# Optimization experiments

Hardware: AMD Instinct MI355X
Metric: run time of the kernel (lower is better)

The kernel has to match this reference:

```python
import jax, jax.numpy as jnp
import numpy as np

HEAD = 8

def setup_inputs() -> dict:
    key = jax.random.key(0)
    ks = jax.random.split(key, 11)
    B, C, W, H = 16, 512, 32, 32
    d, N = C // HEAD, W * H
    return {
        "x": jax.random.normal(ks[0], (B, C, W, H), jnp.float32),
        "Wq": jax.random.normal(ks[1], (C, C), jnp.float32) * 0.02,
        "bq": jax.random.normal(ks[2], (C,), jnp.float32) * 0.02,
        "Wk": jax.random.normal(ks[3], (C, C), jnp.float32) * 0.02,
        "bk": jax.random.normal(ks[4], (C,), jnp.float32) * 0.02,
        "Wv": jax.random.normal(ks[5], (C, C), jnp.float32) * 0.02,
        "bv": jax.random.normal(ks[6], (C,), jnp.float32) * 0.02,
        "rel_h": jax.random.normal(ks[7], (1, HEAD, d, 1, H), jnp.float32),
        "rel_w": jax.random.normal(ks[8], (1, HEAD, d, W, 1), jnp.float32),
        "reg_qk": jax.random.normal(ks[9], (1, N, N), jnp.float32),
        "reg_v": jax.random.normal(ks[10], (1, d, N), jnp.float32),
    }

def reference(x, Wq, bq, Wk, bk, Wv, bv, rel_h, rel_w, reg_qk, reg_v):
    B, C, W, H = x.shape
    head = HEAD
    d = C // head
    N = W * H
    def conv1x1(inp, Wt, b):  # 1x1 conv == per-pixel linear
        return jnp.einsum('bchw,oc->bohw', inp, Wt) + b[None, :, None, None]
    q = conv1x1(x, Wq, bq).reshape(B, head, d, N)
    k = conv1x1(x, Wk, bk).reshape(B, head, d, N)
    v = conv1x1(x, Wv, bv).reshape(B, head, d, N)
    # content-content: q^T k -> [B, head, N, N]
    cc = jnp.einsum('bhdn,bhdm->bhnm', q, k)
    # content-position: (rel_h + rel_w) broadcast to [1, head, d, W, H] -> [head, N, d]
    pos = (rel_h + rel_w).reshape(head, d, N)
    cp = jnp.einsum('hdn,bhdm->bhnm', pos, q)
    energy = cc + cp  # [B, head, N, N]
    n_reg = reg_qk.shape[0]
    energy = jnp.concatenate(
        [energy, jnp.broadcast_to(reg_qk[None], (B, n_reg, N, N))], axis=1)
    v_all = jnp.concatenate(
        [v, jnp.broadcast_to(reg_v[None], (B, n_reg, d, N))], axis=1)
    attn = jax.nn.softmax(energy, axis=-1)  # [B, head+n_reg, N, N]
    # v @ attn^T
    out = jnp.einsum('bgdn,bgmn->bgdm', v_all, attn)
    out = out[:, :head].reshape(B, C, W, H)
    return out + x
```

## Files before the change

### kernel.cpp

```cpp
#include <hip/hip_runtime.h>

#define BB   16
#define HEADS 8
#define DH   64
#define NSP  1024
#define CCH  512

typedef unsigned int   u32;
typedef unsigned short u16;
typedef __attribute__((ext_vector_type(8))) short  short8;
typedef __attribute__((ext_vector_type(4))) float  floatx4;

#if defined(__has_builtin)
#if __has_builtin(__builtin_amdgcn_exp2f)
#define EXP2F(x) __builtin_amdgcn_exp2f(x)
#else
#define EXP2F(x) exp2f(x)
#endif
#else
#define EXP2F(x) exp2f(x)
#endif

__device__ __forceinline__ u16 f2b(float f) {
  u32 x = __float_as_uint(f);
  x = x + 0x7fffu + ((x >> 16) & 1u);
  return (u16)(x >> 16);
}

__device__ __forceinline__ u32 pkbf(float lo, float hi) {
  return __builtin_amdgcn_perm(__float_as_uint(hi) + 0x8000u,
                               __float_as_uint(lo) + 0x8000u, 0x07060302u);
}

__device__ __forceinline__ void gload_lds16(const u16* g, u16* l) {
  __builtin_amdgcn_global_load_lds((const __attribute__((address_space(1))) u32*)g,
                                   (__attribute__((address_space(3))) u32*)l, 16, 0, 0);
}

__global__ __launch_bounds__(256) void prep_wcast(const float* __restrict__ Wq,
                                                  const float* __restrict__ Wk,
                                                  const float* __restrict__ Wv,
                                                  u16* __restrict__ wbf) {
  int idx = blockIdx.x * 256 + threadIdx.x;
  int which = idx >> 16;
  int r4 = (idx & 65535) * 4;
  const float* src = which == 0 ? Wq : which == 1 ? Wk : Wv;
  float4 v = *(const float4*)&src[r4];
  ushort4 s;
  s.x = f2b(v.x); s.y = f2b(v.y); s.z = f2b(v.z); s.w = f2b(v.w);
  *(ushort4*)&wbf[(which << 18) + r4] = s;
}

__global__ __launch_bounds__(256) void prep_pos(const float* __restrict__ rel_h,
                                                const float* __restrict__ rel_w,
                                                u16* __restrict__ pos) {
  int idx = blockIdx.x * 256 + threadIdx.x;
  int dd = idx & 63;
  int n  = (idx >> 6) & 1023;
  int h  = idx >> 16;
  int ww = n >> 5, hh = n & 31;
  float v = rel_h[(h * 64 + dd) * 32 + hh] + rel_w[(h * 64 + dd) * 32 + ww];
  pos[idx] = f2b(v);
}

__global__ __launch_bounds__(256) void prep_xt(const float* __restrict__ x,
                                               u16* __restrict__ xt) {
  int ntile = blockIdx.x, ctile = blockIdx.y, b = blockIdx.z;
  __shared__ float ld[64][68];
  int t = threadIdx.x;
  const float* xb = x + (((size_t)b * CCH + ctile * 64) << 10) + ntile * 64;
#pragma unroll
  for (int p = 0; p < 4; ++p) {
    int c = p * 16 + (t >> 4), n4 = (t & 15) * 4;
    float4 v = *(const float4*)&xb[((size_t)c << 10) + n4];
    ld[c][n4 + 0] = v.x; ld[c][n4 + 1] = v.y; ld[c][n4 + 2] = v.z; ld[c][n4 + 3] = v.w;
  }
  __syncthreads();
  u16* xo = xt + (((size_t)b << 10) + ntile * 64) * CCH + ctile * 64;
#pragma unroll
  for (int p = 0; p < 2; ++p) {
    int id = p * 256 + t;
    int n = id >> 3, c8 = (id & 7) * 8;
    ushort4 s0, s1;
    s0.x = f2b(ld[c8 + 0][n]); s0.y = f2b(ld[c8 + 1][n]);
    s0.z = f2b(ld[c8 + 2][n]); s0.w = f2b(ld[c8 + 3][n]);
    s1.x = f2b(ld[c8 + 4][n]); s1.y = f2b(ld[c8 + 5][n]);
    s1.z = f2b(ld[c8 + 6][n]); s1.w = f2b(ld[c8 + 7][n]);
    *(ushort4*)&xo[(size_t)n * CCH + c8] = s0;
    *(ushort4*)&xo[(size_t)n * CCH + c8 + 4] = s1;
  }
}

__global__ __launch_bounds__(256, 3) void qkv_mfma(const u16* __restrict__ wbf,
                                                   const u16* __restrict__ xt,
                                                   const float* __restrict__ bq,
                                                   const float* __restrict__ bk,
                                                   const float* __restrict__ bv,
                                                   u16* __restrict__ qw,
                                                   u16* __restrict__ kw,
                                                   u16* __restrict__ vtw) {
  int ntile = blockIdx.x, otile = blockIdx.y;
  int b = blockIdx.z & 15, which = blockIdx.z >> 4;
  int o0 = otile * 128, n0 = ntile * 128;

  __shared__ __align__(16) u16 At[128 * 64];
  __shared__ __align__(16) u16 Bt[128 * 64];

  int t = threadIdx.x;
  int w = t >> 6, lane = t & 63;
  int l15 = lane & 15, quad = lane >> 4;
  int wrM = (w >> 1) * 64, wrN = (w & 1) * 64;

  const u16* Ag = wbf + ((size_t)which << 18) + (size_t)o0 * CCH;
  const u16* Bg = xt + (((size_t)b << 10) + n0) * CCH;

  floatx4 acc[4][4];
#pragma unroll
  for (int i = 0; i < 4; ++i)
#pragma unroll
    for (int j = 0; j < 4; ++j) acc[i][j] = (floatx4){0.f, 0.f, 0.f, 0.f};

  const u16* aSrc = which == 2 ? Bt : At;
  const u16* bSrc = which == 2 ? At : Bt;

  int srow = lane >> 3;
  int scc = ((lane & 7) ^ srow) << 3;

  for (int k0 = 0; k0 < CCH; k0 += 64) {
    __syncthreads();
#pragma unroll
    for (int p = 0; p < 4; ++p) {
      int r0 = (w * 4 + p) * 8;
      int row = r0 + srow;
      gload_lds16(Ag + (size_t)row * CCH + k0 + scc, &At[r0 * 64]);
      gload_lds16(Bg + (size_t)row * CCH + k0 + scc, &Bt[r0 * 64]);
    }
    __syncthreads();
#pragma unroll
    for (int ks = 0; ks < 2; ++ks) {
      short8 af[4], bf4[4];
#pragma unroll
      for (int s = 0; s < 4; ++s) {
        int ra = wrM + s * 16 + l15;
        int rb = wrN + s * 16 + l15;
        af[s]  = *(const short8*)&aSrc[ra * 64 + (((ks * 4 + quad) ^ (ra & 7)) << 3)];
        bf4[s] = *(const short8*)&bSrc[rb * 64 + (((ks * 4 + quad) ^ (rb & 7)) << 3)];
      }
#pragma unroll
      for (int i = 0; i < 4; ++i)
#pragma unroll
        for (int j = 0; j < 4; ++j)
          acc[i][j] = __builtin_amdgcn_mfma_f32_16x16x32_bf16(af[i], bf4[j], acc[i][j], 0, 0, 0);
    }
  }

  if (which == 2) {
#pragma unroll
    for (int i = 0; i < 4; ++i) {
      int n = n0 + wrM + i * 16 + quad * 4;
      int nt = n >> 6, nn = n & 63;
#pragma unroll
      for (int j = 0; j < 4; ++j) {
        int o = o0 + wrN + j * 16 + l15;
        int h = o >> 6, dd = o & 63;
        float bias = bv[o];
        uint2 s;
        s.x = pkbf(acc[i][j][0] + bias, acc[i][j][1] + bias);
        s.y = pkbf(acc[i][j][2] + bias, acc[i][j][3] + bias);
        *(uint2*)&vtw[(((size_t)(b * HEADS + h) * 16 + nt) * 64 + dd) * 64 + nn] = s;
      }
    }
  } else {
    const float* bias = which == 0 ? bq : bk;
    u16* dst = which == 0 ? qw : kw;
#pragma unroll
    for (int i = 0; i < 4; ++i) {
      int o = o0 + wrM + i * 16 + quad * 4;
      int h = o >> 6, dd = o & 63;
      float b0 = bias[o], b1 = bias[o + 1], b2 = bias[o + 2], b3 = bias[o + 3];
      size_t hb = (size_t)(b * HEADS + h) * NSP;
#pragma unroll
      for (int j = 0; j < 4; ++j) {
        int n = n0 + wrN + j * 16 + l15;
        uint2 s;
        s.x = pkbf(acc[i][j][0] + b0, acc[i][j][1] + b1);
        s.y = pkbf(acc[i][j][2] + b2, acc[i][j][3] + b3);
        *(uint2*)&dst[(hb + n) * 64 + dd] = s;
      }
    }
  }
}

__global__ __launch_bounds__(256, 2) void attn_mfma(const u16* __restrict__ qw,
                                                    const u16* __restrict__ kw,
                                                    const u16* __restrict__ vtw,
                                                    const u16* __restrict__ pos,
                                                    const float* __restrict__ x,
                                                    float* __restrict__ out) {
  int bh = blockIdx.x, mtile = blockIdx.y;
  int b = bh >> 3, h = bh & 7;
  __shared__ __align__(16) u16 smem_u16[34816];
  u16* pt = smem_u16 + 24576;

  int t = threadIdx.x;
  int w = t >> 6, lane = t & 63;
  int l15 = lane & 15, quad = lane >> 4;
  size_t bhs = (size_t)bh;

  short8 qa[4][2], pa[4][2];
  {
    const short* qg = (const short*)qw + (bhs * NSP + mtile * 256 + w * 64) * 64;
    const short* pg = (const short*)pos + ((size_t)h * NSP + mtile * 256 + w * 64) * 64;
#pragma unroll
    for (int msub = 0; msub < 4; ++msub)
#pragma unroll
      for (int ks = 0; ks < 2; ++ks) {
        int off = (msub * 16 + l15) * 64 + ks * 32 + quad * 8;
        qa[msub][ks] = *(const short8*)(qg + off);
        pa[msub][ks] = *(const short8*)(pg + off);
      }
  }

  floatx4 oacc[4][4];
  float lsum[4] = {0.f, 0.f, 0.f, 0.f};
#pragma unroll
  for (int i = 0; i < 4; ++i)
#pragma unroll
    for (int j = 0; j < 4; ++j) oacc[i][j] = (floatx4){0.f, 0.f, 0.f, 0.f};

  const u16* kg  = kw + bhs * NSP * 64;
  const u16* qgn = qw + bhs * NSP * 64;
  const u16* vg  = vtw + bhs * 16 * 4096;
  u16* ptw = pt + w * 2560;
  int srow = lane >> 3, sc = lane & 7;

  int rs = l15 & 7;
  int c0 = (quad ^ rs) << 3;
  int c1 = ((4 + quad) ^ rs) << 3;

  auto stage = [&](int nt, int buf) {
    u16* kt = smem_u16 + buf * 12288;
    u16* qt = kt + 4096;
    u16* vt = qt + 4096;
#pragma unroll
    for (int p = 0; p < 2; ++p) {
      int r0 = w * 16 + p * 8;
      int row = r0 + srow;
      int swz = ((sc ^ (row & 7)) << 3);
      gload_lds16(kg + (nt * 64 + row) * 64 + swz, &kt[r0 * 64]);
      gload_lds16(qgn + (nt * 64 + row) * 64 + swz, &qt[r0 * 64]);
      gload_lds16(vg + (size_t)nt * 4096 + row * 64 + swz, &vt[r0 * 64]);
    }
  };

  stage(0, 0);

  for (int nt = 0; nt < 16; ++nt) {
    __syncthreads();
    if (nt < 15) stage(nt + 1, (nt + 1) & 1);

    u16* kt = smem_u16 + (nt & 1) * 12288;
    u16* qt = kt + 4096;
    u16* vt = qt + 4096;

#pragma unroll
    for (int half = 0; half < 2; ++half) {
#pragma unroll
      for (int nblk2 = 0; nblk2 < 2; ++nblk2) {
        int nblk = half * 2 + nblk2;
        int rb = (nblk * 16 + l15) * 64;
        short8 kb0 = *(short8*)&kt[rb + c0];
        short8 kb1 = *(short8*)&kt[rb + c1];
        short8 qb0 = *(short8*)&qt[rb + c0];
        short8 qb1 = *(short8*)&qt[rb + c1];
        floatx4 sc4[4];
#pragma unroll
        for (int msub = 0; msub < 4; ++msub) {
          floatx4 c = (floatx4){0.f, 0.f, 0.f, 0.f};
          c = __builtin_amdgcn_mfma_f32_16x16x32_bf16(kb0, qa[msub][0], c, 0, 0, 0);
          c = __builtin_amdgcn_mfma_f32_16x16x32_bf16(kb1, qa[msub][1], c, 0, 0, 0);
          c = __builtin_amdgcn_mfma_f32_16x16x32_bf16(qb0, pa[msub][0], c, 0, 0, 0);
          c = __builtin_amdgcn_mfma_f32_16x16x32_bf16(qb1, pa[msub][1], c, 0, 0, 0);
          sc4[msub] = c;
        }
#pragma unroll
        for (int msub = 0; msub < 4; ++msub) {
          float p0 = EXP2F(fmaf(sc4[msub][0], 1.44269504f, -11.5415603f));
          float p1 = EXP2F(fmaf(sc4[msub][1], 1.44269504f, -11.5415603f));
          float p2 = EXP2F(fmaf(sc4[msub][2], 1.44269504f, -11.5415603f));
          float p3 = EXP2F(fmaf(sc4[msub][3], 1.44269504f, -11.5415603f));
          lsum[msub] += (p0 + p1) + (p2 + p3);
          uint2 pk;
          pk.x = pkbf(p0, p1);
          pk.y = pkbf(p2, p3);
          *(uint2*)&ptw[(msub * 16 + l15) * 40 + nblk2 * 16 + quad * 4] = pk;
        }
      }
      short8 pB[4];
#pragma unroll
      for (int msub = 0; msub < 4; ++msub)
        pB[msub] = *(short8*)&ptw[(msub * 16 + l15) * 40 + quad * 8];
#pragma unroll
      for (int dd = 0; dd < 4; ++dd) {
        int row = dd * 16 + l15;
        short8 vb = *(short8*)&vt[row * 64 + (((half * 4 + quad) ^ (row & 7)) << 3)];
#pragma unroll
        for (int msub = 0; msub < 4; ++msub)
          oacc[msub][dd] = __builtin_amdgcn_mfma_f32_16x16x32_bf16(vb, pB[msub], oacc[msub][dd], 0, 0, 0);
      }
    }
  }

  float rinv[4];
#pragma unroll
  for (int msub = 0; msub < 4; ++msub) {
    float l = lsum[msub];
    l += __shfl_xor(l, 16);
    l += __shfl_xor(l, 32);
    rinv[msub] = 1.0f / l;
  }

  __syncthreads();
  float* ot = (float*)smem_u16 + w * 2304;
  int l8 = lane & 7, lr = lane >> 3;
#pragma unroll
  for (int mh = 0; mh < 2; ++mh) {
#pragma unroll
    for (int ms2 = 0; ms2 < 2; ++ms2) {
      int msub = mh * 2 + ms2;
#pragma unroll
      for (int dd = 0; dd < 4; ++dd)
#pragma unroll
        for (int r = 0; r < 4; ++r)
          ot[(dd * 16 + quad * 4 + r) * 36 + ms2 * 16 + l15] = oacc[msub][dd][r] * rinv[msub];
    }
#pragma unroll
    for (int pass = 0; pass < 8; ++pass) {
      int dd = pass * 8 + lr;
      float4 o4 = *(float4*)&ot[dd * 36 + l8 * 4];
      size_t off = (((size_t)b * CCH + h * DH + dd) << 10) + mtile * 256 + w * 64 + mh * 32 + l8 * 4;
      float4 xv = *(const float4*)&x[off];
      o4.x += xv.x; o4.y += xv.y; o4.z += xv.z; o4.w += xv.w;
      *(float4*)&out[off] = o4;
    }
  }
}

extern "C" void kernel_launch(void* const* d_in, const int* in_sizes, int n_in,
                              void* d_out, int out_size, void* d_ws, size_t ws_size,
                              hipStream_t stream) {
  const float* x     = (const float*)d_in[0];
  const float* Wq    = (const float*)d_in[1];
  const float* bq    = (const float*)d_in[2];
  const float* Wk    = (const float*)d_in[3];
  const float* bk    = (const float*)d_in[4];
  const float* Wv    = (const float*)d_in[5];
  const float* bv    = (const float*)d_in[6];
  const float* rel_h = (const float*)d_in[7];
  const float* rel_w = (const float*)d_in[8];
  float* out = (float*)d_out;

  char* ws = (char*)d_ws;
  u16* qw   = (u16*)(ws);
  u16* kw   = (u16*)(ws + ((size_t)16 << 20));
  u16* vtw  = (u16*)(ws + ((size_t)32 << 20));
  u16* pos  = (u16*)(ws + ((size_t)48 << 20));
  u16* wbf  = (u16*)(ws + ((size_t)49 << 20));
  u16* xt   = (u16*)d_out;

  hipLaunchKernelGGL(prep_wcast, dim3(768), dim3(256), 0, stream, Wq, Wk, Wv, wbf);
  hipLaunchKernelGGL(prep_pos, dim3(2048), dim3(256), 0, stream, rel_h, rel_w, pos);
  hipLaunchKernelGGL(prep_xt, dim3(16, 8, 16), dim3(256), 0, stream, x, xt);
  hipLaunchKernelGGL(qkv_mfma, dim3(8, 4, 48), dim3(256), 0, stream,
                     wbf, xt, bq, bk, bv, qw, kw, vtw);
  hipLaunchKernelGGL(attn_mfma, dim3(128, 4), dim3(256), 0, stream,
                     qw, kw, vtw, pos, x, out);
}
```

Before: 216.1 us.

## Fuse prep kernels into one launch and double-buffer QKV GEMM LDS tiles

Merges the three preprocessing kernels (weight cast, position table, x transpose) into a single launch that dispatches on block index, removing two kernel launches. The QKV projection GEMM now double-buffers its LDS tiles so the next K slice is fetched while the current one is multiplied, with one barrier per iteration instead of two. The LDS footprint doubles and launch bounds drop to 2 blocks per CU, which lowers occupancy. The fused prep kernel reserves the shared array for every block, including the cast and position blocks that never use it.

```diff
diff --git a/kernel.cpp b/kernel.cpp
--- a/kernel.cpp
+++ b/kernel.cpp
@@ -37,61 +37,63 @@
                                    (__attribute__((address_space(3))) u32*)l, 16, 0, 0);
 }
 
-__global__ __launch_bounds__(256) void prep_wcast(const float* __restrict__ Wq,
-                                                  const float* __restrict__ Wk,
-                                                  const float* __restrict__ Wv,
-                                                  u16* __restrict__ wbf) {
-  int idx = blockIdx.x * 256 + threadIdx.x;
-  int which = idx >> 16;
-  int r4 = (idx & 65535) * 4;
-  const float* src = which == 0 ? Wq : which == 1 ? Wk : Wv;
-  float4 v = *(const float4*)&src[r4];
-  ushort4 s;
-  s.x = f2b(v.x); s.y = f2b(v.y); s.z = f2b(v.z); s.w = f2b(v.w);
-  *(ushort4*)&wbf[(which << 18) + r4] = s;
-}
-
-__global__ __launch_bounds__(256) void prep_pos(const float* __restrict__ rel_h,
+__global__ __launch_bounds__(256) void prep_all(const float* __restrict__ x,
+                                                const float* __restrict__ Wq,
+                                                const float* __restrict__ Wk,
+                                                const float* __restrict__ Wv,
+                                                const float* __restrict__ rel_h,
                                                 const float* __restrict__ rel_w,
-                                                u16* __restrict__ pos) {
-  int idx = blockIdx.x * 256 + threadIdx.x;
-  int dd = idx & 63;
-  int n  = (idx >> 6) & 1023;
-  int h  = idx >> 16;
-  int ww = n >> 5, hh = n & 31;
-  float v = rel_h[(h * 64 + dd) * 32 + hh] + rel_w[(h * 64 + dd) * 32 + ww];
-  pos[idx] = f2b(v);
-}
-
-__global__ __launch_bounds__(256) void prep_xt(const float* __restrict__ x,
-                                               u16* __restrict__ xt) {
-  int ntile = blockIdx.x, ctile = blockIdx.y, b = blockIdx.z;
+                                                u16* __restrict__ wbf,
+                                                u16* __restrict__ pos,
+                                                u16* __restrict__ xt) {
   __shared__ float ld[64][68];
+  int bid = blockIdx.x;
   int t = threadIdx.x;
-  const float* xb = x + (((size_t)b * CCH + ctile * 64) << 10) + ntile * 64;
-#pragma unroll
-  for (int p = 0; p < 4; ++p) {
-    int c = p * 16 + (t >> 4), n4 = (t & 15) * 4;
-    float4 v = *(const float4*)&xb[((size_t)c << 10) + n4];
-    ld[c][n4 + 0] = v.x; ld[c][n4 + 1] = v.y; ld[c][n4 + 2] = v.z; ld[c][n4 + 3] = v.w;
-  }
-  __syncthreads();
-  u16* xo = xt + (((size_t)b << 10) + ntile * 64) * CCH + ctile * 64;
-#pragma unroll
-  for (int p = 0; p < 2; ++p) {
-    int id = p * 256 + t;
-    int n = id >> 3, c8 = (id & 7) * 8;
-    ushort4 s0, s1;
-    s0.x = f2b(ld[c8 + 0][n]); s0.y = f2b(ld[c8 + 1][n]);
-    s0.z = f2b(ld[c8 + 2][n]); s0.w = f2b(ld[c8 + 3][n]);
-    s1.x = f2b(ld[c8 + 4][n]); s1.y = f2b(ld[c8 + 5][n]);
-    s1.z = f2b(ld[c8 + 6][n]); s1.w = f2b(ld[c8 + 7][n]);
-    *(ushort4*)&xo[(size_t)n * CCH + c8] = s0;
-    *(ushort4*)&xo[(size_t)n * CCH + c8 + 4] = s1;
-  }
-}
-
-__global__ __launch_bounds__(256, 3) void qkv_mfma(const u16* __restrict__ wbf,
+  if (bid < 768) {
+    int idx = bid * 256 + t;
+    int which = idx >> 16;
+    int r4 = (idx & 65535) * 4;
+    const float* src = which == 0 ? Wq : which == 1 ? Wk : Wv;
+    float4 v = *(const float4*)&src[r4];
+    ushort4 s;
+    s.x = f2b(v.x); s.y = f2b(v.y); s.z = f2b(v.z); s.w = f2b(v.w);
+    *(ushort4*)&wbf[(which << 18) + r4] = s;
+  } else if (bid < 2816) {
+    int idx = (bid - 768) * 256 + t;
+    int dd = idx & 63;
+    int n  = (idx >> 6) & 1023;
+    int h  = idx >> 16;
+    int ww = n >> 5, hh = n & 31;
+    float v = rel_h[(h * 64 + dd) * 32 + hh] + rel_w[(h * 64 + dd) * 32 + ww];
+    pos[idx] = f2b(v);
+  } else {
+    int bid2 = bid - 2816;
+    int ntile = bid2 & 15, ctile = (bid2 >> 4) & 7, b = bid2 >> 7;
+    const float* xb = x + (((size_t)b * CCH + ctile * 64) << 10) + ntile * 64;
+#pragma unroll
+    for (int p = 0; p < 4; ++p) {
+      int c = p * 16 + (t >> 4), n4 = (t & 15) * 4;
+      float4 v = *(const float4*)&xb[((size_t)c << 10) + n4];
+      ld[c][n4 + 0] = v.x; ld[c][n4 + 1] = v.y; ld[c][n4 + 2] = v.z; ld[c][n4 + 3] = v.w;
+    }
+    __syncthreads();
+    u16* xo = xt + (((size_t)b << 10) + ntile * 64) * CCH + ctile * 64;
+#pragma unroll
+    for (int p = 0; p < 2; ++p) {
+      int id = p * 256 + t;
+      int n = id >> 3, c8 = (id & 7) * 8;
+      ushort4 s0, s1;
+      s0.x = f2b(ld[c8 + 0][n]); s0.y = f2b(ld[c8 + 1][n]);
+      s0.z = f2b(ld[c8 + 2][n]); s0.w = f2b(ld[c8 + 3][n]);
+      s1.x = f2b(ld[c8 + 4][n]); s1.y = f2b(ld[c8 + 5][n]);
+      s1.z = f2b(ld[c8 + 6][n]); s1.w = f2b(ld[c8 + 7][n]);
+      *(ushort4*)&xo[(size_t)n * CCH + c8] = s0;
+      *(ushort4*)&xo[(size_t)n * CCH + c8 + 4] = s1;
+    }
+  }
+}
+
+__global__ __launch_bounds__(256, 2) void qkv_mfma(const u16* __restrict__ wbf,
                                                    const u16* __restrict__ xt,
                                                    const float* __restrict__ bq,
                                                    const float* __restrict__ bk,
@@ -103,8 +105,7 @@
   int b = blockIdx.z & 15, which = blockIdx.z >> 4;
   int o0 = otile * 128, n0 = ntile * 128;
 
-  __shared__ __align__(16) u16 At[128 * 64];
-  __shared__ __align__(16) u16 Bt[128 * 64];
+  __shared__ __align__(16) u16 smem[2 * 16384];
 
   int t = threadIdx.x;
   int w = t >> 6, lane = t & 63;
@@ -120,14 +121,12 @@
 #pragma unroll
     for (int j = 0; j < 4; ++j) acc[i][j] = (floatx4){0.f, 0.f, 0.f, 0.f};
 
-  const u16* aSrc = which == 2 ? Bt : At;
-  const u16* bSrc = which == 2 ? At : Bt;
-
   int srow = lane >> 3;
   int scc = ((lane & 7) ^ srow) << 3;
 
-  for (int k0 = 0; k0 < CCH; k0 += 64) {
-    __syncthreads();
+  auto stage = [&](int k0, int buf) {
+    u16* At = smem + buf * 16384;
+    u16* Bt = At + 8192;
 #pragma unroll
     for (int p = 0; p < 4; ++p) {
       int r0 = (w * 4 + p) * 8;
@@ -135,7 +134,19 @@
       gload_lds16(Ag + (size_t)row * CCH + k0 + scc, &At[r0 * 64]);
       gload_lds16(Bg + (size_t)row * CCH + k0 + scc, &Bt[r0 * 64]);
     }
+  };
+
+  stage(0, 0);
+
+  for (int ki = 0; ki < 8; ++ki) {
     __syncthreads();
+    if (ki < 7) stage((ki + 1) * 64, (ki + 1) & 1);
+
+    u16* At = smem + (ki & 1) * 16384;
+    u16* Bt = At + 8192;
+    const u16* aSrc = which == 2 ? Bt : At;
+    const u16* bSrc = which == 2 ? At : Bt;
+
 #pragma unroll
     for (int ks = 0; ks < 2; ++ks) {
       short8 af[4], bf4[4];
@@ -368,9 +379,8 @@
   u16* wbf  = (u16*)(ws + ((size_t)49 << 20));
   u16* xt   = (u16*)d_out;
 
-  hipLaunchKernelGGL(prep_wcast, dim3(768), dim3(256), 0, stream, Wq, Wk, Wv, wbf);
-  hipLaunchKernelGGL(prep_pos, dim3(2048), dim3(256), 0, stream, rel_h, rel_w, pos);
-  hipLaunchKernelGGL(prep_xt, dim3(16, 8, 16), dim3(256), 0, stream, x, xt);
+  hipLaunchKernelGGL(prep_all, dim3(4864), dim3(256), 0, stream,
+                     x, Wq, Wk, Wv, rel_h, rel_w, wbf, pos, xt);
   hipLaunchKernelGGL(qkv_mfma, dim3(8, 4, 48), dim3(256), 0, stream,
                      wbf, xt, bq, bk, bv, qw, kw, vtw);
   hipLaunchKernelGGL(attn_mfma, dim3(128, 4), dim3(256), 0, stream,
```

Measured after the change: 215.7 us. No clear change (-0.2%).
